# Performance work log

Hardware: AMD Instinct MI355X
Metric: run time of the kernel (lower is better)

## Reference

```python
import jax, jax.numpy as jnp
import numpy as np

SPARSITY_RATIO = 0.5

def setup_inputs() -> dict:
    key = jax.random.key(0)
    x = jax.random.normal(key, (32, 128, 128, 128), dtype=jnp.float32)
    return {"x": x}

def reference(x) -> jnp.ndarray:
    B, C, H, W = x.shape
    k = int(SPARSITY_RATIO * H * W)
    absx = jnp.abs(x)
    flat = absx.reshape(B, C, H * W)
    # k-th largest |x| per (b, c) is the threshold
    topvals = jax.lax.top_k(flat, k)[0]          # [B, C, k]
    thresh = topvals[:, :, -1][:, :, None, None]  # [B, C, 1, 1]
    comp = (absx >= thresh).astype(x.dtype)
    return comp * x
```

## Files before the change

### kernel.cpp

```cpp
#include <hip/hip_runtime.h>

#define THREADS 512
#define HW 16384
#define K_SEL 8192u
#define NB1 2048
#define NB2 1024
#define NB3 1024
#define VPT 8

static_assert(THREADS * VPT * 4 == HW, "row tiling");

typedef unsigned uint32x4 __attribute__((ext_vector_type(4)));

template <int NBINS>
__device__ __forceinline__ void find_bin_wave0(const unsigned* __restrict__ hist,
                                               unsigned kRem, unsigned* __restrict__ bc) {
  constexpr int bpl = NBINS >> 6;
  const int lane = (int)(threadIdx.x & 63);
  const int base = lane * bpl;
  unsigned s = 0;
#pragma unroll
  for (int j = 0; j < bpl; ++j) s += hist[base + ((j + lane) & (bpl - 1))];
  unsigned suf = s;
#pragma unroll
  for (int off = 1; off < 64; off <<= 1) {
    unsigned w = __shfl_down(suf, off);
    if (lane + off < 64) suf += w;
  }
  const unsigned cumAbove = suf - s;
  const bool hit = (cumAbove < kRem) && (kRem <= suf);
  const unsigned long long m = __ballot(hit);
  const int tl = (int)__builtin_ctzll(m);
  const unsigned cumTl = __shfl(cumAbove, tl);
  const int j = lane & (bpl - 1);
  const unsigned h = hist[tl * bpl + j];
  unsigned sufc = h;
#pragma unroll
  for (int off = 1; off < 32; off <<= 1) {
    if (off < bpl) {
      unsigned w = __shfl_down(sufc, off);
      if (j + off < bpl) sufc += w;
    }
  }
  const unsigned cumW = sufc - h;
  const bool hit2 = ((cumTl + cumW) < kRem) && (kRem <= cumTl + cumW + h);
  const unsigned long long m2 = __ballot(hit2);
  const int jl = (int)__builtin_ctzll(m2) & (bpl - 1);
  const unsigned kw = __shfl(cumW, jl);
  if (lane == 0) {
    bc[0] = (unsigned)(tl * bpl + jl);
    bc[1] = kRem - cumTl - kw;
  }
}

extern "C" __global__ __launch_bounds__(THREADS, 6)
void sparsify_topk_kernel(const float* __restrict__ x, float* __restrict__ out) {
  __shared__ unsigned h1[NB1];
  __shared__ unsigned h2[NB2];
  __shared__ unsigned h3[NB3];
  __shared__ unsigned bc[2];

  const int t = (int)threadIdx.x;
  const size_t rowOff = (size_t)blockIdx.x * (HW / 4);
  const uint4*    src = (const uint4*)x + rowOff;
  uint32x4*       dst = (uint32x4*)out + rowOff;

  uint4 v[VPT];
#pragma unroll
  for (int i = 0; i < VPT; ++i) v[i] = src[i * THREADS + t];

#pragma unroll
  for (int i = 0; i < NB1 / THREADS; ++i) h1[t + i * THREADS] = 0;
#pragma unroll
  for (int i = 0; i < NB2 / THREADS; ++i) h2[t + i * THREADS] = 0;
#pragma unroll
  for (int i = 0; i < NB3 / THREADS; ++i) h3[t + i * THREADS] = 0;
  __syncthreads();

#pragma unroll
  for (int i = 0; i < VPT; ++i) {
    atomicAdd(&h1[(v[i].x & 0x7fffffffu) >> 20], 1u);
    atomicAdd(&h1[(v[i].y & 0x7fffffffu) >> 20], 1u);
    atomicAdd(&h1[(v[i].z & 0x7fffffffu) >> 20], 1u);
    atomicAdd(&h1[(v[i].w & 0x7fffffffu) >> 20], 1u);
  }
  __syncthreads();
  if (t < 64) find_bin_wave0<NB1>(h1, K_SEL, bc);
  __syncthreads();
  const unsigned T1 = bc[0];
  unsigned kRem = bc[1];

#pragma unroll
  for (int i = 0; i < VPT; ++i) {
    unsigned a;
    a = v[i].x & 0x7fffffffu; if ((a >> 20) == T1) atomicAdd(&h2[(a >> 10) & (NB2 - 1)], 1u);
    a = v[i].y & 0x7fffffffu; if ((a >> 20) == T1) atomicAdd(&h2[(a >> 10) & (NB2 - 1)], 1u);
    a = v[i].z & 0x7fffffffu; if ((a >> 20) == T1) atomicAdd(&h2[(a >> 10) & (NB2 - 1)], 1u);
    a = v[i].w & 0x7fffffffu; if ((a >> 20) == T1) atomicAdd(&h2[(a >> 10) & (NB2 - 1)], 1u);
  }
  __syncthreads();
  if (t < 64) find_bin_wave0<NB2>(h2, kRem, bc);
  __syncthreads();
  const unsigned pref2 = (T1 << 10) | bc[0];
  kRem = bc[1];

#pragma unroll
  for (int i = 0; i < VPT; ++i) {
    unsigned a;
    a = v[i].x & 0x7fffffffu; if ((a >> 10) == pref2) atomicAdd(&h3[a & (NB3 - 1)], 1u);
    a = v[i].y & 0x7fffffffu; if ((a >> 10) == pref2) atomicAdd(&h3[a & (NB3 - 1)], 1u);
    a = v[i].z & 0x7fffffffu; if ((a >> 10) == pref2) atomicAdd(&h3[a & (NB3 - 1)], 1u);
    a = v[i].w & 0x7fffffffu; if ((a >> 10) == pref2) atomicAdd(&h3[a & (NB3 - 1)], 1u);
  }
  __syncthreads();
  if (t < 64) find_bin_wave0<NB3>(h3, kRem, bc);
  __syncthreads();
  const unsigned thr = (pref2 << 10) | bc[0];

#pragma unroll
  for (int i = 0; i < VPT; ++i) {
    uint32x4 w;
    w.x = v[i].x; w.y = v[i].y; w.z = v[i].z; w.w = v[i].w;
    w.x = ((w.x & 0x7fffffffu) >= thr) ? w.x : 0u;
    w.y = ((w.y & 0x7fffffffu) >= thr) ? w.y : 0u;
    w.z = ((w.z & 0x7fffffffu) >= thr) ? w.z : 0u;
    w.w = ((w.w & 0x7fffffffu) >= thr) ? w.w : 0u;
    __builtin_nontemporal_store(w, &dst[i * THREADS + t]);
  }
}

extern "C" void kernel_launch(void* const* d_in, const int* in_sizes, int n_in,
                              void* d_out, int out_size, void* d_ws, size_t ws_size,
                              hipStream_t stream) {
  (void)n_in; (void)d_ws; (void)ws_size; (void)out_size;
  const float* x = (const float*)d_in[0];
  float* out = (float*)d_out;
  const int rows = in_sizes[0] / HW;
  sparsify_topk_kernel<<<dim3(rows), dim3(THREADS), 0, stream>>>(x, out);
}
```

Measured before the change: 103.6 us.

## Stage row in LDS and refine threshold via compact candidate list

Each row is copied into shared memory instead of held in registers, and elements that match the first-level bin are appended to a small candidate list. Later radix passes scan only that list, with finer 7/7/6-bit splits instead of 10/10, and fall back to a full LDS scan if the list overflows. This cuts the per-element work and register pressure of the refinement passes. The cost is about 64KB+ of LDS per block, which limits occupancy for a memory-bound kernel, plus extra LDS round trips and one more histogram pass.

```diff
diff --git a/kernel.cpp b/kernel.cpp
--- a/kernel.cpp
+++ b/kernel.cpp
@@ -4,9 +4,11 @@
 #define HW 16384
 #define K_SEL 8192u
 #define NB1 2048
-#define NB2 1024
-#define NB3 1024
+#define NB2 128
+#define NB3 128
+#define NB4 64
 #define VPT 8
+#define CAP 1024
 
 static_assert(THREADS * VPT * 4 == HW, "row tiling");
 
@@ -32,7 +34,7 @@
   const unsigned long long m = __ballot(hit);
   const int tl = (int)__builtin_ctzll(m);
   const unsigned cumTl = __shfl(cumAbove, tl);
-  const int j = lane & (bpl - 1);
+  const int j = (bpl > 1) ? (lane & (bpl - 1)) : 0;
   const unsigned h = hist[tl * bpl + j];
   unsigned sufc = h;
 #pragma unroll
@@ -45,7 +47,7 @@
   const unsigned cumW = sufc - h;
   const bool hit2 = ((cumTl + cumW) < kRem) && (kRem <= cumTl + cumW + h);
   const unsigned long long m2 = __ballot(hit2);
-  const int jl = (int)__builtin_ctzll(m2) & (bpl - 1);
+  const int jl = (bpl > 1) ? ((int)__builtin_ctzll(m2) & (bpl - 1)) : 0;
   const unsigned kw = __shfl(cumW, jl);
   if (lane == 0) {
     bc[0] = (unsigned)(tl * bpl + jl);
@@ -53,36 +55,39 @@
   }
 }
 
-extern "C" __global__ __launch_bounds__(THREADS, 6)
+extern "C" __global__ __launch_bounds__(THREADS, 4)
 void sparsify_topk_kernel(const float* __restrict__ x, float* __restrict__ out) {
+  __shared__ __align__(16) unsigned data[HW];
   __shared__ unsigned h1[NB1];
   __shared__ unsigned h2[NB2];
   __shared__ unsigned h3[NB3];
+  __shared__ unsigned h4[NB4];
+  __shared__ unsigned list[CAP];
   __shared__ unsigned bc[2];
+  __shared__ unsigned cnt;
 
+  uint4* data4 = (uint4*)data;
   const int t = (int)threadIdx.x;
   const size_t rowOff = (size_t)blockIdx.x * (HW / 4);
   const uint4*    src = (const uint4*)x + rowOff;
   uint32x4*       dst = (uint32x4*)out + rowOff;
 
-  uint4 v[VPT];
-#pragma unroll
-  for (int i = 0; i < VPT; ++i) v[i] = src[i * THREADS + t];
-
 #pragma unroll
   for (int i = 0; i < NB1 / THREADS; ++i) h1[t + i * THREADS] = 0;
-#pragma unroll
-  for (int i = 0; i < NB2 / THREADS; ++i) h2[t + i * THREADS] = 0;
-#pragma unroll
-  for (int i = 0; i < NB3 / THREADS; ++i) h3[t + i * THREADS] = 0;
+  if (t < NB2) h2[t] = 0;
+  if (t < NB3) h3[t] = 0;
+  if (t < NB4) h4[t] = 0;
+  if (t == 0) cnt = 0;
   __syncthreads();
 
 #pragma unroll
   for (int i = 0; i < VPT; ++i) {
-    atomicAdd(&h1[(v[i].x & 0x7fffffffu) >> 20], 1u);
-    atomicAdd(&h1[(v[i].y & 0x7fffffffu) >> 20], 1u);
-    atomicAdd(&h1[(v[i].z & 0x7fffffffu) >> 20], 1u);
-    atomicAdd(&h1[(v[i].w & 0x7fffffffu) >> 20], 1u);
+    const uint4 u = src[i * THREADS + t];
+    data4[i * THREADS + t] = u;
+    atomicAdd(&h1[(u.x & 0x7fffffffu) >> 20], 1u);
+    atomicAdd(&h1[(u.y & 0x7fffffffu) >> 20], 1u);
+    atomicAdd(&h1[(u.z & 0x7fffffffu) >> 20], 1u);
+    atomicAdd(&h1[(u.w & 0x7fffffffu) >> 20], 1u);
   }
   __syncthreads();
   if (t < 64) find_bin_wave0<NB1>(h1, K_SEL, bc);
@@ -91,40 +96,78 @@
   unsigned kRem = bc[1];
 
 #pragma unroll
-  for (int i = 0; i < VPT; ++i) {
+  for (int i = 0; i < HW / 4 / THREADS; ++i) {
+    const uint4 u = data4[i * THREADS + t];
     unsigned a;
-    a = v[i].x & 0x7fffffffu; if ((a >> 20) == T1) atomicAdd(&h2[(a >> 10) & (NB2 - 1)], 1u);
-    a = v[i].y & 0x7fffffffu; if ((a >> 20) == T1) atomicAdd(&h2[(a >> 10) & (NB2 - 1)], 1u);
-    a = v[i].z & 0x7fffffffu; if ((a >> 20) == T1) atomicAdd(&h2[(a >> 10) & (NB2 - 1)], 1u);
-    a = v[i].w & 0x7fffffffu; if ((a >> 20) == T1) atomicAdd(&h2[(a >> 10) & (NB2 - 1)], 1u);
+#define P2_ONE(comp)                                                    \
+    a = u.comp & 0x7fffffffu;                                           \
+    if ((a >> 20) == T1) {                                              \
+      atomicAdd(&h2[(a >> 13) & (NB2 - 1)], 1u);                        \
+      const unsigned idx = atomicAdd(&cnt, 1u);                         \
+      if (idx < CAP) list[idx] = a;                                     \
+    }
+    P2_ONE(x) P2_ONE(y) P2_ONE(z) P2_ONE(w)
+#undef P2_ONE
   }
   __syncthreads();
   if (t < 64) find_bin_wave0<NB2>(h2, kRem, bc);
   __syncthreads();
-  const unsigned pref2 = (T1 << 10) | bc[0];
+  const unsigned pref2 = (T1 << 7) | bc[0];
   kRem = bc[1];
+  const unsigned nC = cnt;
+  const bool fallback = (nC > CAP);
 
+  if (!fallback) {
+    for (unsigned i = t; i < nC; i += THREADS) {
+      const unsigned a = list[i];
+      if ((a >> 13) == pref2) atomicAdd(&h3[(a >> 6) & (NB3 - 1)], 1u);
+    }
+  } else {
 #pragma unroll
-  for (int i = 0; i < VPT; ++i) {
-    unsigned a;
-    a = v[i].x & 0x7fffffffu; if ((a >> 10) == pref2) atomicAdd(&h3[a & (NB3 - 1)], 1u);
-    a = v[i].y & 0x7fffffffu; if ((a >> 10) == pref2) atomicAdd(&h3[a & (NB3 - 1)], 1u);
-    a = v[i].z & 0x7fffffffu; if ((a >> 10) == pref2) atomicAdd(&h3[a & (NB3 - 1)], 1u);
-    a = v[i].w & 0x7fffffffu; if ((a >> 10) == pref2) atomicAdd(&h3[a & (NB3 - 1)], 1u);
+    for (int i = 0; i < HW / 4 / THREADS; ++i) {
+      const uint4 u = data4[i * THREADS + t];
+      unsigned a;
+      a = u.x & 0x7fffffffu; if ((a >> 13) == pref2) atomicAdd(&h3[(a >> 6) & (NB3 - 1)], 1u);
+      a = u.y & 0x7fffffffu; if ((a >> 13) == pref2) atomicAdd(&h3[(a >> 6) & (NB3 - 1)], 1u);
+      a = u.z & 0x7fffffffu; if ((a >> 13) == pref2) atomicAdd(&h3[(a >> 6) & (NB3 - 1)], 1u);
+      a = u.w & 0x7fffffffu; if ((a >> 13) == pref2) atomicAdd(&h3[(a >> 6) & (NB3 - 1)], 1u);
+    }
   }
   __syncthreads();
   if (t < 64) find_bin_wave0<NB3>(h3, kRem, bc);
   __syncthreads();
-  const unsigned thr = (pref2 << 10) | bc[0];
+  const unsigned pref3 = (pref2 << 7) | bc[0];
+  kRem = bc[1];
+
+  if (!fallback) {
+    for (unsigned i = t; i < nC; i += THREADS) {
+      const unsigned a = list[i];
+      if ((a >> 6) == pref3) atomicAdd(&h4[a & (NB4 - 1)], 1u);
+    }
+  } else {
+#pragma unroll
+    for (int i = 0; i < HW / 4 / THREADS; ++i) {
+      const uint4 u = data4[i * THREADS + t];
+      unsigned a;
+      a = u.x & 0x7fffffffu; if ((a >> 6) == pref3) atomicAdd(&h4[a & (NB4 - 1)], 1u);
+      a = u.y & 0x7fffffffu; if ((a >> 6) == pref3) atomicAdd(&h4[a & (NB4 - 1)], 1u);
+      a = u.z & 0x7fffffffu; if ((a >> 6) == pref3) atomicAdd(&h4[a & (NB4 - 1)], 1u);
+      a = u.w & 0x7fffffffu; if ((a >> 6) == pref3) atomicAdd(&h4[a & (NB4 - 1)], 1u);
+    }
+  }
+  __syncthreads();
+  if (t < 64) find_bin_wave0<NB4>(h4, kRem, bc);
+  __syncthreads();
+  const unsigned thr = (pref3 << 6) | bc[0];
 
 #pragma unroll
   for (int i = 0; i < VPT; ++i) {
+    const uint4 u = data4[i * THREADS + t];
     uint32x4 w;
-    w.x = v[i].x; w.y = v[i].y; w.z = v[i].z; w.w = v[i].w;
-    w.x = ((w.x & 0x7fffffffu) >= thr) ? w.x : 0u;
-    w.y = ((w.y & 0x7fffffffu) >= thr) ? w.y : 0u;
-    w.z = ((w.z & 0x7fffffffu) >= thr) ? w.z : 0u;
-    w.w = ((w.w & 0x7fffffffu) >= thr) ? w.w : 0u;
+    w.x = ((u.x & 0x7fffffffu) >= thr) ? u.x : 0u;
+    w.y = ((u.y & 0x7fffffffu) >= thr) ? u.y : 0u;
+    w.z = ((u.z & 0x7fffffffu) >= thr) ? u.z : 0u;
+    w.w = ((u.w & 0x7fffffffu) >= thr) ? u.w : 0u;
     __builtin_nontemporal_store(w, &dst[i * THREADS + t]);
   }
 }
```

Result: slower. 123.8 us (+19.4%).
